# Kernel optimization log

Measured on AMD Instinct MI355X. Metric: run time of the kernel, lower is better.

Reference implementation:

```python
import jax, jax.numpy as jnp
import numpy as np

B, S, D, H = 2, 2048, 1024, 16
DH = D // H

def setup_inputs() -> dict:
    key = jax.random.key(0)
    ks = jax.random.split(key, 12)
    def lin(kw, kb, fan_in):
        bound = 1.0 / np.sqrt(fan_in)
        W = jax.random.uniform(kw, (D, D), jnp.float32, -bound, bound)
        b = jax.random.uniform(kb, (D,), jnp.float32, -bound, bound)
        return W, b
    Wq, bq = lin(ks[0], ks[1], D)
    Wk, bk = lin(ks[2], ks[3], D)
    Wv, bv = lin(ks[4], ks[5], D)
    Wo, bo = lin(ks[6], ks[7], D)
    q = jax.random.normal(ks[8], (B, S, D), jnp.float32)
    k = jax.random.normal(ks[9], (B, S, D), jnp.float32)
    v = jax.random.normal(ks[10], (B, S, D), jnp.float32)
    # causal mask (1 = keep, 0 = masked), broadcastable to [B,H,S,S]
    mask = jnp.tril(jnp.ones((S, S), jnp.int32))[None, None, :, :]
    return {"q": q, "k": k, "v": v, "mask": mask,
            "Wq": Wq, "bq": bq, "Wk": Wk, "bk": bk,
            "Wv": Wv, "bv": bv, "Wo": Wo, "bo": bo}

def reference(q, k, v, mask, Wq, bq, Wk, bk, Wv, bv, Wo, bo):
    # projections: torch Linear is x @ W.T + b
    def split(x):  # [B,S,D] -> [B,H,S,DH]
        return x.reshape(B, S, H, DH).transpose(0, 2, 1, 3)
    qh = split(q @ Wq.T + bq)
    kh = split(k @ Wk.T + bk)
    vh = split(v @ Wv.T + bv)
    score = jnp.einsum('bhqd,bhkd->bhqk', qh, kh) / jnp.sqrt(jnp.float32(DH))
    score = jnp.where(mask == 0, jnp.float32(-1e9), score)
    attn = jax.nn.softmax(score, axis=-1)
    out = jnp.einsum('bhqk,bhkd->bhqd', attn, vh)
    out = out.transpose(0, 2, 1, 3).reshape(B, S, D)
    return out @ Wo.T + bo, attn
```

## Files before the change

kernel.cpp:

```cpp
#include <hip/hip_runtime.h>

#define S_LEN 2048
#define D_MODEL 1024
#define N_HEADS 16
#define D_HEAD 64
#define BATCH 2

typedef __bf16 bf16;
typedef __bf16 bf16x8 __attribute__((ext_vector_type(8)));
typedef __bf16 bf16x4 __attribute__((ext_vector_type(4)));
typedef float f32x4 __attribute__((ext_vector_type(4)));

__device__ __forceinline__ f32x4 mfma16(bf16x8 a, bf16x8 b, f32x4 c) {
  return __builtin_amdgcn_mfma_f32_16x16x32_bf16(a, b, c, 0, 0, 0);
}

__device__ __forceinline__ void gload16(const bf16* g, bf16* lds) {
  __builtin_amdgcn_global_load_lds((const __attribute__((address_space(1))) void*)g,
                                   (__attribute__((address_space(3))) void*)lds, 16, 0, 0);
}

__global__ __launch_bounds__(256) void cvt_w(
    const float* __restrict__ s0, const float* __restrict__ s1,
    const float* __restrict__ s2, const float* __restrict__ s3,
    bf16* __restrict__ d0, bf16* __restrict__ d1, bf16* __restrict__ d2,
    bf16* __restrict__ d3) {
  const int y = blockIdx.y;
  const float* s = (y == 0) ? s0 : (y == 1) ? s1 : (y == 2) ? s2 : s3;
  bf16* d = (y == 0) ? d0 : (y == 1) ? d1 : (y == 2) ? d2 : d3;
  const int i = blockIdx.x * blockDim.x + threadIdx.x;
  const f32x4 a = *(const f32x4*)(s + (size_t)i * 8);
  const f32x4 b = *(const f32x4*)(s + (size_t)i * 8 + 4);
  bf16x8 o;
  o[0] = (bf16)a[0]; o[1] = (bf16)a[1]; o[2] = (bf16)a[2]; o[3] = (bf16)a[3];
  o[4] = (bf16)b[0]; o[5] = (bf16)b[1]; o[6] = (bf16)b[2]; o[7] = (bf16)b[3];
  *(bf16x8*)(d + (size_t)i * 8) = o;
}

__device__ __forceinline__ void gemm_loop(const bf16* __restrict__ gA,
                                          const bf16* __restrict__ gB,
                                          bf16* As, bf16* Bs,
                                          f32x4 (&acc)[4][4], int tid) {
  const int l = tid & 63;
  const int w = tid >> 6;
  const int wr = w >> 1, wc = w & 1;
  const int lr = l & 15, lg = l >> 4;
  const int lrow8 = l >> 3;
  const int colg = ((l & 7) ^ (lrow8 & 7)) * 8;

  for (int k0 = 0; k0 < D_MODEL; k0 += 64) {
#pragma unroll
    for (int i = 0; i < 4; ++i) {
      const int c = w * 4 + i;
      const int row = c * 8 + lrow8;
      gload16(gA + (size_t)row * D_MODEL + k0 + colg, As + c * 512);
      gload16(gB + (size_t)row * D_MODEL + k0 + colg, Bs + c * 512);
    }
    __syncthreads();
#pragma unroll
    for (int half = 0; half < 2; ++half) {
      bf16x8 af[4], bfb[4];
#pragma unroll
      for (int mm = 0; mm < 4; ++mm) {
        const int row = wr * 64 + mm * 16 + lr;
        af[mm] = *(const bf16x8*)(As + row * 64 + ((half * 4 + lg) ^ (lr & 7)) * 8);
      }
#pragma unroll
      for (int nn = 0; nn < 4; ++nn) {
        const int row = wc * 64 + nn * 16 + lr;
        bfb[nn] = *(const bf16x8*)(Bs + row * 64 + ((half * 4 + lg) ^ (lr & 7)) * 8);
      }
#pragma unroll
      for (int mm = 0; mm < 4; ++mm)
#pragma unroll
        for (int nn = 0; nn < 4; ++nn)
          acc[mm][nn] = mfma16(af[mm], bfb[nn], acc[mm][nn]);
    }
    __syncthreads();
  }
}

__device__ __forceinline__ void gemm_loop_af32(const float* __restrict__ gA32,
                                               const bf16* __restrict__ gB,
                                               bf16* As, bf16* Bs,
                                               f32x4 (&acc)[4][4], int tid) {
  const int l = tid & 63;
  const int w = tid >> 6;
  const int wr = w >> 1, wc = w & 1;
  const int lr = l & 15, lg = l >> 4;
  const int lrow8 = l >> 3;
  const int colg = ((l & 7) ^ (lrow8 & 7)) * 8;

  const int arow = tid >> 1;
  const int ahalf = tid & 1;
  const float* aptr = gA32 + (size_t)arow * D_MODEL + ahalf * 32;
  bf16* awr = As + arow * 64;

  for (int k0 = 0; k0 < D_MODEL; k0 += 64) {
    f32x4 av[8];
#pragma unroll
    for (int c = 0; c < 8; ++c) av[c] = *(const f32x4*)(aptr + k0 + c * 4);
#pragma unroll
    for (int i = 0; i < 4; ++i) {
      const int c = w * 4 + i;
      const int row = c * 8 + lrow8;
      gload16(gB + (size_t)row * D_MODEL + k0 + colg, Bs + c * 512);
    }
#pragma unroll
    for (int c8 = 0; c8 < 4; ++c8) {
      bf16x8 o;
#pragma unroll
      for (int e = 0; e < 4; ++e) {
        o[e] = (bf16)av[c8 * 2][e];
        o[e + 4] = (bf16)av[c8 * 2 + 1][e];
      }
      const int col16 = ahalf * 4 + c8;
      *(bf16x8*)(awr + (col16 ^ (arow & 7)) * 8) = o;
    }
    __syncthreads();
#pragma unroll
    for (int half = 0; half < 2; ++half) {
      bf16x8 af[4], bfb[4];
#pragma unroll
      for (int mm = 0; mm < 4; ++mm) {
        const int row = wr * 64 + mm * 16 + lr;
        af[mm] = *(const bf16x8*)(As + row * 64 + ((half * 4 + lg) ^ (lr & 7)) * 8);
      }
#pragma unroll
      for (int nn = 0; nn < 4; ++nn) {
        const int row = wc * 64 + nn * 16 + lr;
        bfb[nn] = *(const bf16x8*)(Bs + row * 64 + ((half * 4 + lg) ^ (lr & 7)) * 8);
      }
#pragma unroll
      for (int mm = 0; mm < 4; ++mm)
#pragma unroll
        for (int nn = 0; nn < 4; ++nn)
          acc[mm][nn] = mfma16(af[mm], bfb[nn], acc[mm][nn]);
    }
    __syncthreads();
  }
}

__global__ __launch_bounds__(256) void gemm_qkv(
    const float* __restrict__ qf, const float* __restrict__ kf,
    const float* __restrict__ vf, const bf16* __restrict__ Wqb,
    const bf16* __restrict__ Wkb, const bf16* __restrict__ Wvb,
    const float* __restrict__ biasq, const float* __restrict__ biask,
    const float* __restrict__ biasv, bf16* __restrict__ qhw,
    bf16* __restrict__ khw, bf16* __restrict__ vtw) {
  __shared__ bf16 As[128 * 64];
  __shared__ bf16 Bs[128 * 64];
  __shared__ bf16 T[128][72];
  const int z = blockIdx.z;
  const float* A = (z == 0) ? qf : (z == 1) ? kf : vf;
  const bf16* W = (z == 0) ? Wqb : (z == 1) ? Wkb : Wvb;
  const float* bias = (z == 0) ? biasq : (z == 1) ? biask : biasv;
  const float scale = (z == 0) ? 0.125f : 1.0f;
  bf16* out = (z == 0) ? qhw : (z == 1) ? khw : vtw;

  const int tid = threadIdx.x;
  const int l = tid & 63;
  const int w = tid >> 6;
  const int wr = w >> 1, wc = w & 1;
  const int lr = l & 15, lg = l >> 4;

  f32x4 acc[4][4] = {};
  gemm_loop_af32(A + ((size_t)blockIdx.x * 128) * D_MODEL,
                 W + ((size_t)blockIdx.y * 128) * D_MODEL, As, Bs, acc, tid);

  const int b = (blockIdx.x * 128) >> 11;
  const int s0 = (blockIdx.x * 128) & 2047;

  if (z == 2) {
#pragma unroll
    for (int half = 0; half < 2; ++half) {
      if (wc == half) {
#pragma unroll
        for (int nn = 0; nn < 4; ++nn) {
          const int n = blockIdx.y * 128 + half * 64 + nn * 16 + lr;
          const float bv = bias[n];
#pragma unroll
          for (int mm = 0; mm < 4; ++mm)
#pragma unroll
            for (int r = 0; r < 4; ++r) {
              const int ml = wr * 64 + mm * 16 + lg * 4 + r;
              T[ml][nn * 16 + lr] = (bf16)(acc[mm][nn][r] + bv);
            }
        }
      }
      __syncthreads();
      const int d = tid & 63;
      const int sblk = (tid >> 6) * 32;
      const int hglob = blockIdx.y * 2 + half;
      bf16* orow = vtw + (((size_t)(b * N_HEADS + hglob)) * D_HEAD + d) * S_LEN + s0 + sblk;
#pragma unroll
      for (int j = 0; j < 4; ++j) {
        bf16x8 pk;
#pragma unroll
        for (int e = 0; e < 8; ++e) pk[e] = T[sblk + j * 8 + e][d];
        *(bf16x8*)(orow + j * 8) = pk;
      }
      __syncthreads();
    }
  } else {
#pragma unroll
    for (int half = 0; half < 2; ++half) {
      if (wc == half) {
#pragma unroll
        for (int nn = 0; nn < 4; ++nn) {
          const int n = blockIdx.y * 128 + half * 64 + nn * 16 + lr;
          const float bv = bias[n];
#pragma unroll
          for (int mm = 0; mm < 4; ++mm)
#pragma unroll
            for (int r = 0; r < 4; ++r) {
              const int ml = wr * 64 + mm * 16 + lg * 4 + r;
              T[ml][nn * 16 + lr] = (bf16)((acc[mm][nn][r] + bv) * scale);
            }
        }
      }
      __syncthreads();
      const int hglob = blockIdx.y * 2 + half;
      bf16* obase = out + ((size_t)(b * N_HEADS + hglob) * S_LEN + s0) * D_HEAD;
      const int rsub = tid >> 3;
      const int d8 = (tid & 7) * 8;
#pragma unroll
      for (int j = 0; j < 4; ++j) {
        const int row_l = j * 32 + rsub;
        *(bf16x8*)(obase + (size_t)row_l * D_HEAD + d8) = *(const bf16x8*)(&T[row_l][d8]);
      }
      __syncthreads();
    }
  }
}

__device__ __forceinline__ void stage_strip(const bf16* __restrict__ src,
                                            size_t rstride, bf16* lds, int tid) {
#pragma unroll
  for (int rnd = 0; rnd < 2; ++rnd) {
    const int chunk = rnd * 256 + tid;
    const int row = chunk >> 3;
    const int c8 = chunk & 7;
    const int src8 = c8 ^ (row & 7);
    gload16(src + (size_t)row * rstride + src8 * 8, lds + chunk * 8);
  }
}

__global__ __launch_bounds__(256) void attn_flash(
    const bf16* __restrict__ qh, const bf16* __restrict__ kh,
    const bf16* __restrict__ vt, bf16* __restrict__ ctx,
    float* __restrict__ lbuf, float* __restrict__ attn) {
  __shared__ bf16 Kb[2][64 * 64];
  __shared__ bf16 Vb[2][64 * 64];
  __shared__ bf16 P[4][16][72];
  const int tid = threadIdx.x;
  const int w = tid >> 6, l = tid & 63;
  const int lr = l & 15, lg = l >> 4;
  const int bh = blockIdx.y;
  const int bxx = blockIdx.x;

  if (bxx >= 32) {
    int rem = bxx - 32, zq = 0, cnt = 7;
    while (rem >= cnt) { rem -= cnt; --cnt; ++zq; }
    const int kq = zq + 1 + rem;
    float* base = attn + (size_t)bh * S_LEN * S_LEN + (size_t)(zq * 256) * S_LEN + kq * 256;
    const f32x4 zv = {};
    for (int it = 0; it < 64; ++it) {
      float* rp = base + (size_t)(it * 4 + w) * S_LEN + l * 4;
      __builtin_nontemporal_store(zv, (f32x4*)rp);
    }
    return;
  }

  const int qgroup = (bxx & 1) ? (31 - (bxx >> 1)) : (bxx >> 1);
  const int q0 = qgroup * 64 + w * 16;
  const int qrow = q0 + lr;
  const bf16* qp = qh + (size_t)bh * S_LEN * D_HEAD;
  const bf16* kp = kh + (size_t)bh * S_LEN * D_HEAD;
  const bf16* vp = vt + (size_t)bh * D_HEAD * S_LEN;

  const bf16x8 qf0 = *(const bf16x8*)(qp + (size_t)qrow * D_HEAD + lg * 8);
  const bf16x8 qf1 = *(const bf16x8*)(qp + (size_t)qrow * D_HEAD + 32 + lg * 8);

  const float NINF = -__builtin_inff();
  const int nfull = qgroup;
  const int x0 = (lg ^ (lr & 7)) * 8;
  const int x1 = ((4 | lg) ^ (lr & 7)) * 8;

  stage_strip(kp, D_HEAD, Kb[0], tid);
  stage_strip(vp, S_LEN, Vb[0], tid);
  __syncthreads();

  float lsum = 0.f;
  f32x4 oacc[4] = {};
  int cur = 0;

  for (int st = 0; st < nfull; ++st) {
    stage_strip(kp + (size_t)(st + 1) * 64 * D_HEAD, D_HEAD, Kb[cur ^ 1], tid);
    stage_strip(vp + (st + 1) * 64, S_LEN, Vb[cur ^ 1], tid);

    float ps = 0.f;
    __builtin_amdgcn_s_setprio(1);
    f32x4 zz4[4];
#pragma unroll
    for (int t = 0; t < 4; ++t) {
      const bf16* krow = Kb[cur] + (t * 16 + lr) * 64;
      f32x4 zz = {};
      zz = mfma16(*(const bf16x8*)(krow + x0), qf0, zz);
      zz = mfma16(*(const bf16x8*)(krow + x1), qf1, zz);
      zz4[t] = zz;
    }
    __builtin_amdgcn_s_setprio(0);
#pragma unroll
    for (int t = 0; t < 4; ++t) {
      bf16x4 pk;
#pragma unroll
      for (int r = 0; r < 4; ++r) {
        const float e = __expf(fminf(zz4[t][r], 60.f));
        ps += e;
        pk[r] = (bf16)e;
      }
      *(bf16x4*)(&P[w][lr][t * 16 + lg * 4]) = pk;
    }
    ps += __shfl_xor(ps, 16);
    ps += __shfl_xor(ps, 32);
    lsum += ps;
    const bf16x8 pb0 = *(const bf16x8*)(&P[w][lr][lg * 8]);
    const bf16x8 pb1 = *(const bf16x8*)(&P[w][lr][32 + lg * 8]);
    __builtin_amdgcn_s_setprio(1);
#pragma unroll
    for (int dt = 0; dt < 4; ++dt) {
      const bf16* vrow = Vb[cur] + (dt * 16 + lr) * 64;
      oacc[dt] = mfma16(*(const bf16x8*)(vrow + x0), pb0, oacc[dt]);
      oacc[dt] = mfma16(*(const bf16x8*)(vrow + x1), pb1, oacc[dt]);
    }
    __builtin_amdgcn_s_setprio(0);
    __syncthreads();
    cur ^= 1;
  }

  {
    float ps = 0.f;
#pragma unroll
    for (int t = 0; t < 4; ++t) {
      bf16x4 pk;
      if (t <= w) {
        const bf16* krow = Kb[cur] + (t * 16 + lr) * 64;
        f32x4 zz = {};
        zz = mfma16(*(const bf16x8*)(krow + x0), qf0, zz);
        zz = mfma16(*(const bf16x8*)(krow + x1), qf1, zz);
#pragma unroll
        for (int r = 0; r < 4; ++r) {
          const float sv = (t == w && (lg * 4 + r) > lr) ? NINF : zz[r];
          const float e = __expf(fminf(sv, 60.f));
          ps += e;
          pk[r] = (bf16)e;
        }
      } else {
#pragma unroll
        for (int r = 0; r < 4; ++r) pk[r] = (bf16)0.f;
      }
      *(bf16x4*)(&P[w][lr][t * 16 + lg * 4]) = pk;
    }
    ps += __shfl_xor(ps, 16);
    ps += __shfl_xor(ps, 32);
    lsum += ps;
    const bf16x8 pb0 = *(const bf16x8*)(&P[w][lr][lg * 8]);
    const bf16x8 pb1 = *(const bf16x8*)(&P[w][lr][32 + lg * 8]);
#pragma unroll
    for (int dt = 0; dt < 4; ++dt) {
      const bf16* vrow = Vb[cur] + (dt * 16 + lr) * 64;
      oacc[dt] = mfma16(*(const bf16x8*)(vrow + x0), pb0, oacc[dt]);
      oacc[dt] = mfma16(*(const bf16x8*)(vrow + x1), pb1, oacc[dt]);
    }
  }

  const float invl = 1.0f / lsum;
  const int b = bh >> 4, h = bh & 15;
  bf16* crow = ctx + ((size_t)(b * S_LEN + qrow)) * D_MODEL + h * D_HEAD;
#pragma unroll
  for (int dt = 0; dt < 4; ++dt) {
    bf16x4 ov;
#pragma unroll
    for (int r = 0; r < 4; ++r) ov[r] = (bf16)(oacc[dt][r] * invl);
    *(bf16x4*)(crow + dt * 16 + lg * 4) = ov;
  }
  if (lg == 0) lbuf[(size_t)bh * S_LEN + qrow] = invl;
}

__global__ __launch_bounds__(256) void mat_out(
    const bf16* __restrict__ qh, const bf16* __restrict__ kh,
    const float* __restrict__ lbuf, float* __restrict__ attn,
    const bf16* __restrict__ ctxA, const bf16* __restrict__ Wo,
    const float* __restrict__ bo, float* __restrict__ outp) {
  __shared__ __align__(16) char smem[34048];
  const int bid = blockIdx.x;
  const int tid = threadIdx.x;
  const int w = tid >> 6, l = tid & 63;
  const int lr = l & 15, lg = l >> 4;

  if (bid < 256) {
    bf16* As = (bf16*)smem;
    bf16* Bs = (bf16*)(smem + 16384);
    const int bx = bid & 31, by = bid >> 5;
    const int wr = w >> 1, wc = w & 1;
    f32x4 acc[4][4] = {};
    gemm_loop(ctxA + ((size_t)bx * 128) * D_MODEL,
              Wo + ((size_t)by * 128) * D_MODEL, As, Bs, acc, tid);
    const int rowg0 = bx * 128 + wr * 64;
    const int colg0 = by * 128 + wc * 64;
#pragma unroll
    for (int nn = 0; nn < 4; ++nn) {
      const int n = colg0 + nn * 16 + lr;
      const float bv = bo[n];
#pragma unroll
      for (int mm = 0; mm < 4; ++mm)
#pragma unroll
        for (int r = 0; r < 4; ++r) {
          const int m = rowg0 + mm * 16 + lg * 4 + r;
          __builtin_nontemporal_store(acc[mm][nn][r] + bv,
                                      outp + (size_t)m * D_MODEL + n);
        }
    }
    return;
  }

  bf16* Pt = (bf16*)smem;
  const int mid = bid - 256;
  const int bh = mid / 144;
  int rem = mid - bh * 144;
  int g = 0;
  while (2 * (g + 1) * (g + 2) <= rem) ++g;
  const int rem2 = rem - 2 * g * (g + 1);
  const int q0t = 4 * g + rem2 / (g + 1);
  const int kq = rem2 - (g + 1) * (rem2 / (g + 1));
  const int q0 = q0t * 64;
  const int k0b = kq * 256;
  float* ap = attn + (size_t)bh * S_LEN * S_LEN;

  const int k0 = k0b + w * 64;
  if (k0 <= q0 + 63) {
    const bf16* qp = qh + (size_t)bh * S_LEN * D_HEAD;
    const bf16* kp = kh + (size_t)bh * S_LEN * D_HEAD;
    float iv[4];
#pragma unroll
    for (int qs = 0; qs < 4; ++qs)
      iv[qs] = lbuf[(size_t)bh * S_LEN + q0 + qs * 16 + lr];
    bf16x8 kf[4][2], qf[4][2];
#pragma unroll
    for (int kt = 0; kt < 4; ++kt) {
      kf[kt][0] = *(const bf16x8*)(kp + (size_t)(k0 + kt * 16 + lr) * D_HEAD + lg * 8);
      kf[kt][1] = *(const bf16x8*)(kp + (size_t)(k0 + kt * 16 + lr) * D_HEAD + 32 + lg * 8);
    }
#pragma unroll
    for (int qs = 0; qs < 4; ++qs) {
      qf[qs][0] = *(const bf16x8*)(qp + (size_t)(q0 + qs * 16 + lr) * D_HEAD + lg * 8);
      qf[qs][1] = *(const bf16x8*)(qp + (size_t)(q0 + qs * 16 + lr) * D_HEAD + 32 + lg * 8);
    }
    f32x4 acc[4][4] = {};
#pragma unroll
    for (int qs = 0; qs < 4; ++qs)
#pragma unroll
      for (int kt = 0; kt < 4; ++kt) {
        acc[qs][kt] = mfma16(kf[kt][0], qf[qs][0], acc[qs][kt]);
        acc[qs][kt] = mfma16(kf[kt][1], qf[qs][1], acc[qs][kt]);
      }
#pragma unroll
    for (int qs = 0; qs < 4; ++qs) {
      const int q = q0 + qs * 16 + lr;
#pragma unroll
      for (int kt = 0; kt < 4; ++kt) {
        const int kbase = k0 + kt * 16 + lg * 4;
        bf16x4 pk;
#pragma unroll
        for (int r = 0; r < 4; ++r) {
          const float pv = (kbase + r > q)
                               ? 0.f
                               : __expf(fminf(acc[qs][kt][r], 60.f)) * iv[qs];
          pk[r] = (bf16)pv;
        }
        *(bf16x4*)(Pt + (qs * 16 + lr) * 264 + w * 64 + kt * 16 + lg * 4) = pk;
      }
    }
  } else {
    const bf16x4 z4 = {};
#pragma unroll
    for (int j = 0; j < 16; ++j)
      *(bf16x4*)(Pt + (j * 4 + lg) * 264 + w * 64 + lr * 4) = z4;
  }
  __syncthreads();

#pragma unroll
  for (int j = 0; j < 16; ++j) {
    const int rowl = w * 16 + j;
    const bf16x4 pk = *(const bf16x4*)(Pt + rowl * 264 + l * 4);
    f32x4 o;
    o[0] = (float)pk[0]; o[1] = (float)pk[1];
    o[2] = (float)pk[2]; o[3] = (float)pk[3];
    __builtin_nontemporal_store(
        o, (f32x4*)(ap + (size_t)(q0 + rowl) * S_LEN + k0b + l * 4));
  }
}

extern "C" void kernel_launch(void* const* d_in, const int* in_sizes, int n_in,
                              void* d_out, int out_size, void* d_ws, size_t ws_size,
                              hipStream_t stream) {
  (void)in_sizes; (void)n_in; (void)out_size; (void)ws_size;
  const float* q  = (const float*)d_in[0];
  const float* k  = (const float*)d_in[1];
  const float* v  = (const float*)d_in[2];
  const float* Wq = (const float*)d_in[4];
  const float* bq = (const float*)d_in[5];
  const float* Wk = (const float*)d_in[6];
  const float* bk = (const float*)d_in[7];
  const float* Wv = (const float*)d_in[8];
  const float* bv = (const float*)d_in[9];
  const float* Wo = (const float*)d_in[10];
  const float* bo = (const float*)d_in[11];

  float* outp = (float*)d_out;
  float* attn = outp + (size_t)BATCH * S_LEN * D_MODEL;

  char* ws = (char*)d_ws;
  bf16* qhw  = (bf16*)(ws);
  bf16* khw  = (bf16*)(ws + (8u << 20));
  bf16* vtw  = (bf16*)(ws + (16u << 20));
  bf16* ctxb = (bf16*)(ws + (24u << 20));
  bf16* Wqb  = (bf16*)(ws + (32u << 20));
  bf16* Wkb  = (bf16*)(ws + (34u << 20));
  bf16* Wvb  = (bf16*)(ws + (36u << 20));
  bf16* Wob  = (bf16*)(ws + (38u << 20));
  float* lbuf = (float*)(ws + (40u << 20));

  dim3 bb(256);
  cvt_w<<<dim3(512, 4), bb, 0, stream>>>(Wq, Wk, Wv, Wo, Wqb, Wkb, Wvb, Wob);
  gemm_qkv<<<dim3(32, 8, 3), bb, 0, stream>>>(q, k, v, Wqb, Wkb, Wvb,
                                              bq, bk, bv, qhw, khw, vtw);
  attn_flash<<<dim3(60, 32), bb, 0, stream>>>(qhw, khw, vtw, ctxb, lbuf, attn);
  mat_out<<<dim3(256 + 4608), bb, 0, stream>>>(qhw, khw, lbuf, attn,
                                               ctxb, Wob, bo, outp);
}
```

Measured before the change: 266.9 us.

## Split attention into row-sum pass and fused PV pass that writes probabilities

After: 277.9 us. +4.1%, slower.

```diff
diff --git a/kernel.cpp b/kernel.cpp
--- a/kernel.cpp
+++ b/kernel.cpp
@@ -246,10 +246,88 @@
   }
 }
 
-__global__ __launch_bounds__(256) void attn_flash(
+__global__ __launch_bounds__(256) void attn_lsum(
     const bf16* __restrict__ qh, const bf16* __restrict__ kh,
-    const bf16* __restrict__ vt, bf16* __restrict__ ctx,
-    float* __restrict__ lbuf, float* __restrict__ attn) {
+    float* __restrict__ lbuf) {
+  __shared__ bf16 Kb[2][64 * 64];
+  const int tid = threadIdx.x;
+  const int w = tid >> 6, l = tid & 63;
+  const int lr = l & 15, lg = l >> 4;
+  const int bh = blockIdx.y;
+  const int bxx = blockIdx.x;
+  const int qgroup = (bxx & 1) ? (31 - (bxx >> 1)) : (bxx >> 1);
+  const int q0 = qgroup * 64 + w * 16;
+  const int qrow = q0 + lr;
+  const bf16* qp = qh + (size_t)bh * S_LEN * D_HEAD;
+  const bf16* kp = kh + (size_t)bh * S_LEN * D_HEAD;
+
+  const bf16x8 qf0 = *(const bf16x8*)(qp + (size_t)qrow * D_HEAD + lg * 8);
+  const bf16x8 qf1 = *(const bf16x8*)(qp + (size_t)qrow * D_HEAD + 32 + lg * 8);
+
+  const float NINF = -__builtin_inff();
+  const int nfull = qgroup;
+  const int x0 = (lg ^ (lr & 7)) * 8;
+  const int x1 = ((4 | lg) ^ (lr & 7)) * 8;
+
+  stage_strip(kp, D_HEAD, Kb[0], tid);
+  __syncthreads();
+
+  float lsum = 0.f;
+  int cur = 0;
+
+  for (int st = 0; st < nfull; ++st) {
+    stage_strip(kp + (size_t)(st + 1) * 64 * D_HEAD, D_HEAD, Kb[cur ^ 1], tid);
+    float ps = 0.f;
+    __builtin_amdgcn_s_setprio(1);
+    f32x4 zz4[4];
+#pragma unroll
+    for (int t = 0; t < 4; ++t) {
+      const bf16* krow = Kb[cur] + (t * 16 + lr) * 64;
+      f32x4 zz = {};
+      zz = mfma16(*(const bf16x8*)(krow + x0), qf0, zz);
+      zz = mfma16(*(const bf16x8*)(krow + x1), qf1, zz);
+      zz4[t] = zz;
+    }
+    __builtin_amdgcn_s_setprio(0);
+#pragma unroll
+    for (int t = 0; t < 4; ++t)
+#pragma unroll
+      for (int r = 0; r < 4; ++r) ps += __expf(fminf(zz4[t][r], 60.f));
+    ps += __shfl_xor(ps, 16);
+    ps += __shfl_xor(ps, 32);
+    lsum += ps;
+    __syncthreads();
+    cur ^= 1;
+  }
+
+  {
+    float ps = 0.f;
+#pragma unroll
+    for (int t = 0; t < 4; ++t) {
+      if (t <= w) {
+        const bf16* krow = Kb[cur] + (t * 16 + lr) * 64;
+        f32x4 zz = {};
+        zz = mfma16(*(const bf16x8*)(krow + x0), qf0, zz);
+        zz = mfma16(*(const bf16x8*)(krow + x1), qf1, zz);
+#pragma unroll
+        for (int r = 0; r < 4; ++r) {
+          const float sv = (t == w && (lg * 4 + r) > lr) ? NINF : zz[r];
+          ps += __expf(fminf(sv, 60.f));
+        }
+      }
+    }
+    ps += __shfl_xor(ps, 16);
+    ps += __shfl_xor(ps, 32);
+    lsum += ps;
+  }
+
+  if (lg == 0) lbuf[(size_t)bh * S_LEN + qrow] = 1.0f / lsum;
+}
+
+__global__ __launch_bounds__(256) void attn_pv(
+    const bf16* __restrict__ qh, const bf16* __restrict__ kh,
+    const bf16* __restrict__ vt, const float* __restrict__ lbuf,
+    bf16* __restrict__ ctx, float* __restrict__ attn) {
   __shared__ bf16 Kb[2][64 * 64];
   __shared__ bf16 Vb[2][64 * 64];
   __shared__ bf16 P[4][16][72];
@@ -278,12 +356,15 @@
   const bf16* qp = qh + (size_t)bh * S_LEN * D_HEAD;
   const bf16* kp = kh + (size_t)bh * S_LEN * D_HEAD;
   const bf16* vp = vt + (size_t)bh * D_HEAD * S_LEN;
+  float* ap = attn + (size_t)bh * S_LEN * S_LEN;
 
   const bf16x8 qf0 = *(const bf16x8*)(qp + (size_t)qrow * D_HEAD + lg * 8);
   const bf16x8 qf1 = *(const bf16x8*)(qp + (size_t)qrow * D_HEAD + 32 + lg * 8);
+  const float invl = lbuf[(size_t)bh * S_LEN + qrow];
 
   const float NINF = -__builtin_inff();
   const int nfull = qgroup;
+  const int ktail = ((qgroup >> 2) << 2) + 4;
   const int x0 = (lg ^ (lr & 7)) * 8;
   const int x1 = ((4 | lg) ^ (lr & 7)) * 8;
 
@@ -291,7 +372,6 @@
   stage_strip(vp, S_LEN, Vb[0], tid);
   __syncthreads();
 
-  float lsum = 0.f;
   f32x4 oacc[4] = {};
   int cur = 0;
 
@@ -299,7 +379,6 @@
     stage_strip(kp + (size_t)(st + 1) * 64 * D_HEAD, D_HEAD, Kb[cur ^ 1], tid);
     stage_strip(vp + (st + 1) * 64, S_LEN, Vb[cur ^ 1], tid);
 
-    float ps = 0.f;
     __builtin_amdgcn_s_setprio(1);
     f32x4 zz4[4];
 #pragma unroll
@@ -315,16 +394,10 @@
     for (int t = 0; t < 4; ++t) {
       bf16x4 pk;
 #pragma unroll
-      for (int r = 0; r < 4; ++r) {
-        const float e = __expf(fminf(zz4[t][r], 60.f));
-        ps += e;
-        pk[r] = (bf16)e;
-      }
+      for (int r = 0; r < 4; ++r)
+        pk[r] = (bf16)(__expf(fminf(zz4[t][r], 60.f)) * invl);
       *(bf16x4*)(&P[w][lr][t * 16 + lg * 4]) = pk;
     }
-    ps += __shfl_xor(ps, 16);
-    ps += __shfl_xor(ps, 32);
-    lsum += ps;
     const bf16x8 pb0 = *(const bf16x8*)(&P[w][lr][lg * 8]);
     const bf16x8 pb1 = *(const bf16x8*)(&P[w][lr][32 + lg * 8]);
     __builtin_amdgcn_s_setprio(1);
@@ -335,12 +408,22 @@
       oacc[dt] = mfma16(*(const bf16x8*)(vrow + x1), pb1, oacc[dt]);
     }
     __builtin_amdgcn_s_setprio(0);
+#pragma unroll
+    for (int j = 0; j < 4; ++j) {
+      const int row = j * 4 + lg;
+      const bf16x4 pk4 = *(const bf16x4*)(&P[w][row][lr * 4]);
+      f32x4 o;
+      o[0] = (float)pk4[0]; o[1] = (float)pk4[1];
+      o[2] = (float)pk4[2]; o[3] = (float)pk4[3];
+      __builtin_nontemporal_store(
+          o, (f32x4*)(ap + (size_t)(q0 + row) * S_LEN + st * 64 + lr * 4));
+    }
     __syncthreads();
     cur ^= 1;
   }
 
   {
-    float ps = 0.f;
+    const int st = nfull;
 #pragma unroll
     for (int t = 0; t < 4; ++t) {
       bf16x4 pk;
@@ -352,9 +435,7 @@
 #pragma unroll
         for (int r = 0; r < 4; ++r) {
           const float sv = (t == w && (lg * 4 + r) > lr) ? NINF : zz[r];
-          const float e = __expf(fminf(sv, 60.f));
-          ps += e;
-          pk[r] = (bf16)e;
+          pk[r] = (bf16)(__expf(fminf(sv, 60.f)) * invl);
         }
       } else {
 #pragma unroll
@@ -362,9 +443,6 @@
       }
       *(bf16x4*)(&P[w][lr][t * 16 + lg * 4]) = pk;
     }
-    ps += __shfl_xor(ps, 16);
-    ps += __shfl_xor(ps, 32);
-    lsum += ps;
     const bf16x8 pb0 = *(const bf16x8*)(&P[w][lr][lg * 8]);
     const bf16x8 pb1 = *(const bf16x8*)(&P[w][lr][32 + lg * 8]);
 #pragma unroll
@@ -373,132 +451,69 @@
       oacc[dt] = mfma16(*(const bf16x8*)(vrow + x0), pb0, oacc[dt]);
       oacc[dt] = mfma16(*(const bf16x8*)(vrow + x1), pb1, oacc[dt]);
     }
-  }
-
-  const float invl = 1.0f / lsum;
+#pragma unroll
+    for (int j = 0; j < 4; ++j) {
+      const int row = j * 4 + lg;
+      const bf16x4 pk4 = *(const bf16x4*)(&P[w][row][lr * 4]);
+      f32x4 o;
+      o[0] = (float)pk4[0]; o[1] = (float)pk4[1];
+      o[2] = (float)pk4[2]; o[3] = (float)pk4[3];
+      __builtin_nontemporal_store(
+          o, (f32x4*)(ap + (size_t)(q0 + row) * S_LEN + st * 64 + lr * 4));
+    }
+  }
+
+  for (int st = nfull + 1; st < ktail; ++st) {
+    const f32x4 zv = {};
+#pragma unroll
+    for (int j = 0; j < 4; ++j) {
+      const int row = j * 4 + lg;
+      __builtin_nontemporal_store(
+          zv, (f32x4*)(ap + (size_t)(q0 + row) * S_LEN + st * 64 + lr * 4));
+    }
+  }
+
   const int b = bh >> 4, h = bh & 15;
   bf16* crow = ctx + ((size_t)(b * S_LEN + qrow)) * D_MODEL + h * D_HEAD;
 #pragma unroll
   for (int dt = 0; dt < 4; ++dt) {
     bf16x4 ov;
 #pragma unroll
-    for (int r = 0; r < 4; ++r) ov[r] = (bf16)(oacc[dt][r] * invl);
+    for (int r = 0; r < 4; ++r) ov[r] = (bf16)oacc[dt][r];
     *(bf16x4*)(crow + dt * 16 + lg * 4) = ov;
   }
-  if (lg == 0) lbuf[(size_t)bh * S_LEN + qrow] = invl;
-}
-
-__global__ __launch_bounds__(256) void mat_out(
-    const bf16* __restrict__ qh, const bf16* __restrict__ kh,
-    const float* __restrict__ lbuf, float* __restrict__ attn,
-    const bf16* __restrict__ ctxA, const bf16* __restrict__ Wo,
-    const float* __restrict__ bo, float* __restrict__ outp) {
-  __shared__ __align__(16) char smem[34048];
-  const int bid = blockIdx.x;
+}
+
+__global__ __launch_bounds__(256) void gemm_out(const bf16* __restrict__ A,
+                                                const bf16* __restrict__ W,
+                                                const float* __restrict__ bias,
+                                                float* __restrict__ out) {
+  __shared__ bf16 As[128 * 64];
+  __shared__ bf16 Bs[128 * 64];
   const int tid = threadIdx.x;
-  const int w = tid >> 6, l = tid & 63;
+  const int l = tid & 63;
+  const int w = tid >> 6;
+  const int wr = w >> 1, wc = w & 1;
   const int lr = l & 15, lg = l >> 4;
 
-  if (bid < 256) {
-    bf16* As = (bf16*)smem;
-    bf16* Bs = (bf16*)(smem + 16384);
-    const int bx = bid & 31, by = bid >> 5;
-    const int wr = w >> 1, wc = w & 1;
-    f32x4 acc[4][4] = {};
-    gemm_loop(ctxA + ((size_t)bx * 128) * D_MODEL,
-              Wo + ((size_t)by * 128) * D_MODEL, As, Bs, acc, tid);
-    const int rowg0 = bx * 128 + wr * 64;
-    const int colg0 = by * 128 + wc * 64;
-#pragma unroll
-    for (int nn = 0; nn < 4; ++nn) {
-      const int n = colg0 + nn * 16 + lr;
-      const float bv = bo[n];
-#pragma unroll
-      for (int mm = 0; mm < 4; ++mm)
-#pragma unroll
-        for (int r = 0; r < 4; ++r) {
-          const int m = rowg0 + mm * 16 + lg * 4 + r;
-          __builtin_nontemporal_store(acc[mm][nn][r] + bv,
-                                      outp + (size_t)m * D_MODEL + n);
-        }
-    }
-    return;
-  }
-
-  bf16* Pt = (bf16*)smem;
-  const int mid = bid - 256;
-  const int bh = mid / 144;
-  int rem = mid - bh * 144;
-  int g = 0;
-  while (2 * (g + 1) * (g + 2) <= rem) ++g;
-  const int rem2 = rem - 2 * g * (g + 1);
-  const int q0t = 4 * g + rem2 / (g + 1);
-  const int kq = rem2 - (g + 1) * (rem2 / (g + 1));
-  const int q0 = q0t * 64;
-  const int k0b = kq * 256;
-  float* ap = attn + (size_t)bh * S_LEN * S_LEN;
-
-  const int k0 = k0b + w * 64;
-  if (k0 <= q0 + 63) {
-    const bf16* qp = qh + (size_t)bh * S_LEN * D_HEAD;
-    const bf16* kp = kh + (size_t)bh * S_LEN * D_HEAD;
-    float iv[4];
-#pragma unroll
-    for (int qs = 0; qs < 4; ++qs)
-      iv[qs] = lbuf[(size_t)bh * S_LEN + q0 + qs * 16 + lr];
-    bf16x8 kf[4][2], qf[4][2];
-#pragma unroll
-    for (int kt = 0; kt < 4; ++kt) {
-      kf[kt][0] = *(const bf16x8*)(kp + (size_t)(k0 + kt * 16 + lr) * D_HEAD + lg * 8);
-      kf[kt][1] = *(const bf16x8*)(kp + (size_t)(k0 + kt * 16 + lr) * D_HEAD + 32 + lg * 8);
-    }
-#pragma unroll
-    for (int qs = 0; qs < 4; ++qs) {
-      qf[qs][0] = *(const bf16x8*)(qp + (size_t)(q0 + qs * 16 + lr) * D_HEAD + lg * 8);
-      qf[qs][1] = *(const bf16x8*)(qp + (size_t)(q0 + qs * 16 + lr) * D_HEAD + 32 + lg * 8);
-    }
-    f32x4 acc[4][4] = {};
-#pragma unroll
-    for (int qs = 0; qs < 4; ++qs)
-#pragma unroll
-      for (int kt = 0; kt < 4; ++kt) {
-        acc[qs][kt] = mfma16(kf[kt][0], qf[qs][0], acc[qs][kt]);
-        acc[qs][kt] = mfma16(kf[kt][1], qf[qs][1], acc[qs][kt]);
-      }
-#pragma unroll
-    for (int qs = 0; qs < 4; ++qs) {
-      const int q = q0 + qs * 16 + lr;
-#pragma unroll
-      for (int kt = 0; kt < 4; ++kt) {
-        const int kbase = k0 + kt * 16 + lg * 4;
-        bf16x4 pk;
-#pragma unroll
-        for (int r = 0; r < 4; ++r) {
-          const float pv = (kbase + r > q)
-                               ? 0.f
-                               : __expf(fminf(acc[qs][kt][r], 60.f)) * iv[qs];
-          pk[r] = (bf16)pv;
-        }
-        *(bf16x4*)(Pt + (qs * 16 + lr) * 264 + w * 64 + kt * 16 + lg * 4) = pk;
-      }
-    }
-  } else {
-    const bf16x4 z4 = {};
-#pragma unroll
-    for (int j = 0; j < 16; ++j)
-      *(bf16x4*)(Pt + (j * 4 + lg) * 264 + w * 64 + lr * 4) = z4;
-  }
-  __syncthreads();
-
-#pragma unroll
-  for (int j = 0; j < 16; ++j) {
-    const int rowl = w * 16 + j;
-    const bf16x4 pk = *(const bf16x4*)(Pt + rowl * 264 + l * 4);
-    f32x4 o;
-    o[0] = (float)pk[0]; o[1] = (float)pk[1];
-    o[2] = (float)pk[2]; o[3] = (float)pk[3];
-    __builtin_nontemporal_store(
-        o, (f32x4*)(ap + (size_t)(q0 + rowl) * S_LEN + k0b + l * 4));
+  f32x4 acc[4][4] = {};
+  gemm_loop(A + ((size_t)blockIdx.x * 128) * D_MODEL,
+            W + ((size_t)blockIdx.y * 128) * D_MODEL, As, Bs, acc, tid);
+
+  const int rowg0 = blockIdx.x * 128 + wr * 64;
+  const int colg0 = blockIdx.y * 128 + wc * 64;
+#pragma unroll
+  for (int nn = 0; nn < 4; ++nn) {
+    const int n = colg0 + nn * 16 + lr;
+    const float bv = bias[n];
+#pragma unroll
+    for (int mm = 0; mm < 4; ++mm)
+#pragma unroll
+      for (int r = 0; r < 4; ++r) {
+        const int m = rowg0 + mm * 16 + lg * 4 + r;
+        __builtin_nontemporal_store(acc[mm][nn][r] + bv,
+                                    out + (size_t)m * D_MODEL + n);
+      }
   }
 }
 
@@ -536,7 +551,7 @@
   cvt_w<<<dim3(512, 4), bb, 0, stream>>>(Wq, Wk, Wv, Wo, Wqb, Wkb, Wvb, Wob);
   gemm_qkv<<<dim3(32, 8, 3), bb, 0, stream>>>(q, k, v, Wqb, Wkb, Wvb,
                                               bq, bk, bv, qhw, khw, vtw);
-  attn_flash<<<dim3(60, 32), bb, 0, stream>>>(qhw, khw, vtw, ctxb, lbuf, attn);
-  mat_out<<<dim3(256 + 4608), bb, 0, stream>>>(qhw, khw, lbuf, attn,
-                                               ctxb, Wob, bo, outp);
-}
+  attn_lsum<<<dim3(32, 32), bb, 0, stream>>>(qhw, khw, lbuf);
+  attn_pv<<<dim3(60, 32), bb, 0, stream>>>(qhw, khw, vtw, lbuf, ctxb, attn);
+  gemm_out<<<dim3(32, 8), bb, 0, stream>>>(ctxb, Wob, bo, outp);
+}
```

## Double-buffer GEMM K-loop with BK=32 stages and prefetch next tile

Applied to the files above, without the earlier changes.

Result: faster. 236.6 us (-11.3%).

```diff
diff --git a/kernel.cpp b/kernel.cpp
--- a/kernel.cpp
+++ b/kernel.cpp
@@ -45,39 +45,44 @@
   const int w = tid >> 6;
   const int wr = w >> 1, wc = w & 1;
   const int lr = l & 15, lg = l >> 4;
-  const int lrow8 = l >> 3;
-  const int colg = ((l & 7) ^ (lrow8 & 7)) * 8;
-
-  for (int k0 = 0; k0 < D_MODEL; k0 += 64) {
-#pragma unroll
-    for (int i = 0; i < 4; ++i) {
-      const int c = w * 4 + i;
-      const int row = c * 8 + lrow8;
-      gload16(gA + (size_t)row * D_MODEL + k0 + colg, As + c * 512);
-      gload16(gB + (size_t)row * D_MODEL + k0 + colg, Bs + c * 512);
-    }
+  const int rl = l >> 2;
+  const int c8l = l & 3;
+  const int chA = lg ^ ((lr >> 1) & 3);
+
+#define STAGE_PAIR(ks, buf)                                                   \
+  {                                                                           \
+    _Pragma("unroll") for (int i = 0; i < 2; ++i) {                           \
+      const int blk = w + i * 4;                                              \
+      const int row = blk * 16 + rl;                                          \
+      const int s8 = c8l ^ ((row >> 1) & 3);                                  \
+      gload16(gA + (size_t)row * D_MODEL + (ks) * 32 + s8 * 8,                \
+              As + (buf) * 4096 + blk * 512);                                 \
+      gload16(gB + (size_t)row * D_MODEL + (ks) * 32 + s8 * 8,                \
+              Bs + (buf) * 4096 + blk * 512);                                 \
+    }                                                                         \
+  }
+
+  STAGE_PAIR(0, 0);
+  __syncthreads();
+  int cur = 0;
+  for (int ks = 0; ks < 32; ++ks) {
+    if (ks < 31) STAGE_PAIR(ks + 1, cur ^ 1);
+    bf16x8 af[4], bfb[4];
+#pragma unroll
+    for (int mm = 0; mm < 4; ++mm)
+      af[mm] = *(const bf16x8*)(As + cur * 4096 + (wr * 64 + mm * 16 + lr) * 32 + chA * 8);
+#pragma unroll
+    for (int nn = 0; nn < 4; ++nn)
+      bfb[nn] = *(const bf16x8*)(Bs + cur * 4096 + (wc * 64 + nn * 16 + lr) * 32 + chA * 8);
+#pragma unroll
+    for (int mm = 0; mm < 4; ++mm)
+#pragma unroll
+      for (int nn = 0; nn < 4; ++nn)
+        acc[mm][nn] = mfma16(af[mm], bfb[nn], acc[mm][nn]);
     __syncthreads();
-#pragma unroll
-    for (int half = 0; half < 2; ++half) {
-      bf16x8 af[4], bfb[4];
-#pragma unroll
-      for (int mm = 0; mm < 4; ++mm) {
-        const int row = wr * 64 + mm * 16 + lr;
-        af[mm] = *(const bf16x8*)(As + row * 64 + ((half * 4 + lg) ^ (lr & 7)) * 8);
-      }
-#pragma unroll
-      for (int nn = 0; nn < 4; ++nn) {
-        const int row = wc * 64 + nn * 16 + lr;
-        bfb[nn] = *(const bf16x8*)(Bs + row * 64 + ((half * 4 + lg) ^ (lr & 7)) * 8);
-      }
-#pragma unroll
-      for (int mm = 0; mm < 4; ++mm)
-#pragma unroll
-        for (int nn = 0; nn < 4; ++nn)
-          acc[mm][nn] = mfma16(af[mm], bfb[nn], acc[mm][nn]);
-    }
-    __syncthreads();
-  }
+    cur ^= 1;
+  }
+#undef STAGE_PAIR
 }
 
 __device__ __forceinline__ void gemm_loop_af32(const float* __restrict__ gA32,
@@ -88,57 +93,75 @@
   const int w = tid >> 6;
   const int wr = w >> 1, wc = w & 1;
   const int lr = l & 15, lg = l >> 4;
-  const int lrow8 = l >> 3;
-  const int colg = ((l & 7) ^ (lrow8 & 7)) * 8;
+  const int rl = l >> 2, c8l = l & 3;
+  const int chA = lg ^ ((lr >> 1) & 3);
 
   const int arow = tid >> 1;
   const int ahalf = tid & 1;
-  const float* aptr = gA32 + (size_t)arow * D_MODEL + ahalf * 32;
-  bf16* awr = As + arow * 64;
-
-  for (int k0 = 0; k0 < D_MODEL; k0 += 64) {
-    f32x4 av[8];
-#pragma unroll
-    for (int c = 0; c < 8; ++c) av[c] = *(const f32x4*)(aptr + k0 + c * 4);
-#pragma unroll
-    for (int i = 0; i < 4; ++i) {
-      const int c = w * 4 + i;
-      const int row = c * 8 + lrow8;
-      gload16(gB + (size_t)row * D_MODEL + k0 + colg, Bs + c * 512);
-    }
-#pragma unroll
-    for (int c8 = 0; c8 < 4; ++c8) {
-      bf16x8 o;
-#pragma unroll
-      for (int e = 0; e < 4; ++e) {
-        o[e] = (bf16)av[c8 * 2][e];
-        o[e + 4] = (bf16)av[c8 * 2 + 1][e];
-      }
-      const int col16 = ahalf * 4 + c8;
-      *(bf16x8*)(awr + (col16 ^ (arow & 7)) * 8) = o;
-    }
+  const float* aptr = gA32 + (size_t)arow * D_MODEL + ahalf * 16;
+  const int asw = (arow >> 1) & 3;
+
+#define LOAD_A(ks, av)                                                        \
+  _Pragma("unroll") for (int c = 0; c < 4; ++c)                               \
+      av[c] = *(const f32x4*)(aptr + (ks) * 32 + c * 4);
+
+#define WRITE_A(buf, av)                                                      \
+  {                                                                           \
+    _Pragma("unroll") for (int j = 0; j < 2; ++j) {                           \
+      bf16x8 o;                                                               \
+      _Pragma("unroll") for (int e = 0; e < 4; ++e) {                         \
+        o[e] = (bf16)av[j * 2][e];                                            \
+        o[e + 4] = (bf16)av[j * 2 + 1][e];                                    \
+      }                                                                       \
+      const int c8 = ahalf * 2 + j;                                           \
+      *(bf16x8*)(As + (buf) * 4096 + arow * 32 + (c8 ^ asw) * 8) = o;         \
+    }                                                                         \
+  }
+
+#define STAGE_B(ks, buf)                                                      \
+  {                                                                           \
+    _Pragma("unroll") for (int i = 0; i < 2; ++i) {                           \
+      const int blk = w + i * 4;                                              \
+      const int row = blk * 16 + rl;                                          \
+      const int s8 = c8l ^ ((row >> 1) & 3);                                  \
+      gload16(gB + (size_t)row * D_MODEL + (ks) * 32 + s8 * 8,                \
+              Bs + (buf) * 4096 + blk * 512);                                 \
+    }                                                                         \
+  }
+
+  {
+    f32x4 av[4];
+    LOAD_A(0, av);
+    STAGE_B(0, 0);
+    WRITE_A(0, av);
+  }
+  __syncthreads();
+  int cur = 0;
+  for (int ks = 0; ks < 32; ++ks) {
+    f32x4 av[4];
+    if (ks < 31) {
+      LOAD_A(ks + 1, av);
+      STAGE_B(ks + 1, cur ^ 1);
+    }
+    bf16x8 af[4], bfb[4];
+#pragma unroll
+    for (int mm = 0; mm < 4; ++mm)
+      af[mm] = *(const bf16x8*)(As + cur * 4096 + (wr * 64 + mm * 16 + lr) * 32 + chA * 8);
+#pragma unroll
+    for (int nn = 0; nn < 4; ++nn)
+      bfb[nn] = *(const bf16x8*)(Bs + cur * 4096 + (wc * 64 + nn * 16 + lr) * 32 + chA * 8);
+#pragma unroll
+    for (int mm = 0; mm < 4; ++mm)
+#pragma unroll
+      for (int nn = 0; nn < 4; ++nn)
+        acc[mm][nn] = mfma16(af[mm], bfb[nn], acc[mm][nn]);
+    if (ks < 31) WRITE_A(cur ^ 1, av);
     __syncthreads();
-#pragma unroll
-    for (int half = 0; half < 2; ++half) {
-      bf16x8 af[4], bfb[4];
-#pragma unroll
-      for (int mm = 0; mm < 4; ++mm) {
-        const int row = wr * 64 + mm * 16 + lr;
-        af[mm] = *(const bf16x8*)(As + row * 64 + ((half * 4 + lg) ^ (lr & 7)) * 8);
-      }
-#pragma unroll
-      for (int nn = 0; nn < 4; ++nn) {
-        const int row = wc * 64 + nn * 16 + lr;
-        bfb[nn] = *(const bf16x8*)(Bs + row * 64 + ((half * 4 + lg) ^ (lr & 7)) * 8);
-      }
-#pragma unroll
-      for (int mm = 0; mm < 4; ++mm)
-#pragma unroll
-        for (int nn = 0; nn < 4; ++nn)
-          acc[mm][nn] = mfma16(af[mm], bfb[nn], acc[mm][nn]);
-    }
-    __syncthreads();
-  }
+    cur ^= 1;
+  }
+#undef LOAD_A
+#undef WRITE_A
+#undef STAGE_B
 }
 
 __global__ __launch_bounds__(256) void gemm_qkv(
@@ -148,9 +171,11 @@
     const float* __restrict__ biasq, const float* __restrict__ biask,
     const float* __restrict__ biasv, bf16* __restrict__ qhw,
     bf16* __restrict__ khw, bf16* __restrict__ vtw) {
-  __shared__ bf16 As[128 * 64];
-  __shared__ bf16 Bs[128 * 64];
-  __shared__ bf16 T[128][72];
+  __shared__ __align__(16) char smem[32768];
+  bf16* As = (bf16*)smem;
+  bf16* Bs = (bf16*)(smem + 16384);
+  typedef bf16 Trow[72];
+  Trow* T = (Trow*)smem;
   const int z = blockIdx.z;
   const float* A = (z == 0) ? qf : (z == 1) ? kf : vf;
   const bf16* W = (z == 0) ? Wqb : (z == 1) ? Wkb : Wvb;
```
